# Performance work log

Hardware: AMD Instinct MI355X
Metric: run time of the kernel (lower is better)

## Reference

```python
import jax, jax.numpy as jnp
import numpy as np

N_USER, N_ITEM, N_REL = 200000, 100000, 64
DIM = 64
S_UU = S_UI = S_IU = S_II = 8
BATCH = 65536
MAX_RATING = 5.0


def setup_inputs() -> dict:
    key = jax.random.key(0)
    ks = jax.random.split(key, 24)
    inp = {}
    # query batch
    inp['u'] = jax.random.randint(ks[0], (BATCH,), 0, N_USER)
    inp['v'] = jax.random.randint(ks[1], (BATCH,), 0, N_ITEM)
    # embedding tables (init std=0.8 as in the torch code)
    inp['usr_feat'] = 0.8 * jax.random.normal(ks[2], (N_USER, DIM), jnp.float32)
    inp['item_feat'] = 0.8 * jax.random.normal(ks[3], (N_ITEM, DIM), jnp.float32)
    inp['rel_feat'] = 0.8 * jax.random.normal(ks[4], (N_REL, DIM), jnp.float32)
    # precomputed sampled neighbor tables (built once in __init__ in the original)
    inp['neigh_uu'] = jax.random.randint(ks[5], (N_USER, S_UU), 0, N_USER)
    inp['neigh_uu_st'] = jax.random.uniform(ks[6], (N_USER, S_UU), jnp.float32)
    inp['neigh_ui'] = jax.random.randint(ks[7], (N_USER, S_UI), 0, N_ITEM)
    inp['neigh_ui_rat'] = MAX_RATING * jax.random.uniform(ks[8], (N_USER, S_UI), jnp.float32)
    inp['neigh_ui_vot'] = jax.random.uniform(ks[9], (N_USER, S_UI), jnp.float32)
    inp['neigh_ui_tim'] = jax.random.uniform(ks[10], (N_USER, S_UI), jnp.float32)
    inp['neigh_iu'] = jax.random.randint(ks[11], (N_ITEM, S_IU), 0, N_USER)
    inp['neigh_iu_rat'] = MAX_RATING * jax.random.uniform(ks[12], (N_ITEM, S_IU), jnp.float32)
    inp['neigh_iu_vot'] = jax.random.uniform(ks[13], (N_ITEM, S_IU), jnp.float32)
    inp['neigh_iu_tim'] = jax.random.uniform(ks[14], (N_ITEM, S_IU), jnp.float32)
    inp['neigh_ii'] = jax.random.randint(ks[15], (N_ITEM, S_II), 0, N_ITEM)
    inp['neigh_ir'] = jax.random.randint(ks[16], (N_ITEM, S_II), 0, N_REL)
    # aggregator transforms (one per side)
    sc = 1.0 / np.sqrt(DIM)
    inp['Wu'] = sc * jax.random.normal(ks[17], (DIM, DIM), jnp.float32)
    inp['bu'] = jnp.zeros((DIM,), jnp.float32)
    inp['Wv'] = sc * jax.random.normal(ks[18], (DIM, DIM), jnp.float32)
    inp['bv'] = jnp.zeros((DIM,), jnp.float32)
    return inp


def reference(u, v, usr_feat, item_feat, rel_feat,
              neigh_uu, neigh_uu_st, neigh_ui, neigh_ui_rat, neigh_ui_vot, neigh_ui_tim,
              neigh_iu, neigh_iu_rat, neigh_iu_vot, neigh_iu_tim, neigh_ii, neigh_ir,
              Wu, bu, Wv, bv):
    u_emb = usr_feat[u]                                   # [B, D]
    v_emb = item_feat[v]                                  # [B, D]

    # ---- user-side aggregation ----
    # social neighbors, weighted by softmax over social tie strength
    uu_nei = usr_feat[neigh_uu[u]]                        # [B, S, D]
    w_uu = jax.nn.softmax(neigh_uu_st[u], axis=-1)        # [B, S]
    agg_uu = jnp.einsum('bs,bsd->bd', w_uu, uu_nei)
    # interacted items, weighted by rating * vote * time recency
    ui_nei = item_feat[neigh_ui[u]]                       # [B, S, D]
    s_ui = neigh_ui_rat[u] * neigh_ui_vot[u] * neigh_ui_tim[u]
    w_ui = jax.nn.softmax(s_ui, axis=-1)
    agg_ui = jnp.einsum('bs,bsd->bd', w_ui, ui_nei)
    user_h = jax.nn.relu((u_emb + agg_uu + agg_ui) @ Wu + bu)

    # ---- item-side aggregation ----
    # users who interacted with the item, weighted like above
    iu_nei = usr_feat[neigh_iu[v]]                        # [B, S, D]
    s_iu = neigh_iu_rat[v] * neigh_iu_vot[v] * neigh_iu_tim[v]
    w_iu = jax.nn.softmax(s_iu, axis=-1)
    agg_iu = jnp.einsum('bs,bsd->bd', w_iu, iu_nei)
    # KG neighbors with user-relation attention (KGCN-style)
    ii_nei = item_feat[neigh_ii[v]]                       # [B, S, D]
    rel = rel_feat[neigh_ir[v]]                           # [B, S, D]
    att = jnp.einsum('bd,bsd->bs', u_emb, rel)            # user-relation score
    w_ii = jax.nn.softmax(att, axis=-1)
    agg_ii = jnp.einsum('bs,bsd->bd', w_ii, ii_nei)
    item_h = jax.nn.relu((v_emb + agg_iu + agg_ii) @ Wv + bv)

    # rating prediction
    score = jax.nn.sigmoid(jnp.sum(user_h * item_h, axis=-1)) * MAX_RATING
    return score
```

## Files before the change

### kernel.cpp

```cpp
#include <hip/hip_runtime.h>
#include <math.h>

constexpr int DIM = 64;
constexpr int S = 8;
constexpr int WPB = 4;
constexpr int BLOCK = WPB * 64;
constexpr int GRID = 1024;

typedef __attribute__((ext_vector_type(8))) __bf16 bf16x8;
typedef __attribute__((ext_vector_type(4))) float  f32x4;

#define LDS_FENCE() asm volatile("s_waitcnt lgkmcnt(0)" ::: "memory")

template <int CTRL>
__device__ __forceinline__ float dppx(float x) {
    return __builtin_bit_cast(float,
        __builtin_amdgcn_mov_dpp(__builtin_bit_cast(int, x), CTRL, 0xf, 0xf, true));
}
#define XOR1 0xB1
#define XOR2 0x4E

__device__ __forceinline__ unsigned pk_bf16(float a, float b) {
    unsigned ua = __builtin_bit_cast(unsigned, a);
    unsigned ub = __builtin_bit_cast(unsigned, b);
    ua = (ua + 0x8000u) >> 16;
    ub = (ub + 0x8000u) & 0xffff0000u;
    return ua | ub;
}

__device__ __forceinline__ void octet_softmax(float sc, float* wout) {
    float m = sc;
    m = fmaxf(m, dppx<XOR1>(m));
    m = fmaxf(m, dppx<XOR2>(m));
    m = fmaxf(m, __shfl_xor(m, 4));
    float e = __expf(sc - m);
    float s = e;
    s += dppx<XOR1>(s);
    s += dppx<XOR2>(s);
    s += __shfl_xor(s, 4);
    float w = e / s;
    #pragma unroll
    for (int k = 0; k < 8; k++) wout[k] = __shfl(w, k);
}

__device__ __forceinline__ void matvec_h(
    float xv, int lane, unsigned short* xw,
    const bf16x8* xa00, const bf16x8* xa01,
    const bf16x8* xa10, const bf16x8* xa11,
    const unsigned* bf,
    float b0, float b1, float b2, float b3,
    float& h0, float& h1, float& h2, float& h3)
{
    LDS_FENCE();
    const unsigned xb = __builtin_bit_cast(unsigned, xv);
    const unsigned hb = (xb + 0x8000u) & 0xffff0000u;
    const float xl = xv - __builtin_bit_cast(float, hb);
    xw[lane]      = (unsigned short)(hb >> 16);
    xw[64 + lane] = (unsigned short)((__builtin_bit_cast(unsigned, xl) + 0x8000u) >> 16);
    LDS_FENCE();

    f32x4 a0 = {0.f, 0.f, 0.f, 0.f};
    f32x4 a1 = a0, a2 = a0, a3 = a0;

    {
        const bf16x8 ah = *xa00, al = *xa01;
        const bf16x8 w0 = *(const bf16x8*)(bf);
        const bf16x8 w1 = *(const bf16x8*)(bf + 256);
        const bf16x8 w2 = *(const bf16x8*)(bf + 512);
        const bf16x8 w3 = *(const bf16x8*)(bf + 768);
        a0 = __builtin_amdgcn_mfma_f32_16x16x32_bf16(ah, w0, a0, 0, 0, 0);
        a0 = __builtin_amdgcn_mfma_f32_16x16x32_bf16(al, w0, a0, 0, 0, 0);
        a1 = __builtin_amdgcn_mfma_f32_16x16x32_bf16(ah, w1, a1, 0, 0, 0);
        a1 = __builtin_amdgcn_mfma_f32_16x16x32_bf16(al, w1, a1, 0, 0, 0);
        a2 = __builtin_amdgcn_mfma_f32_16x16x32_bf16(ah, w2, a2, 0, 0, 0);
        a2 = __builtin_amdgcn_mfma_f32_16x16x32_bf16(al, w2, a2, 0, 0, 0);
        a3 = __builtin_amdgcn_mfma_f32_16x16x32_bf16(ah, w3, a3, 0, 0, 0);
        a3 = __builtin_amdgcn_mfma_f32_16x16x32_bf16(al, w3, a3, 0, 0, 0);
    }
    {
        const bf16x8 ah = *xa10, al = *xa11;
        const bf16x8 w0 = *(const bf16x8*)(bf + 1024);
        const bf16x8 w1 = *(const bf16x8*)(bf + 1280);
        const bf16x8 w2 = *(const bf16x8*)(bf + 1536);
        const bf16x8 w3 = *(const bf16x8*)(bf + 1792);
        a0 = __builtin_amdgcn_mfma_f32_16x16x32_bf16(ah, w0, a0, 0, 0, 0);
        a0 = __builtin_amdgcn_mfma_f32_16x16x32_bf16(al, w0, a0, 0, 0, 0);
        a1 = __builtin_amdgcn_mfma_f32_16x16x32_bf16(ah, w1, a1, 0, 0, 0);
        a1 = __builtin_amdgcn_mfma_f32_16x16x32_bf16(al, w1, a1, 0, 0, 0);
        a2 = __builtin_amdgcn_mfma_f32_16x16x32_bf16(ah, w2, a2, 0, 0, 0);
        a2 = __builtin_amdgcn_mfma_f32_16x16x32_bf16(al, w2, a2, 0, 0, 0);
        a3 = __builtin_amdgcn_mfma_f32_16x16x32_bf16(ah, w3, a3, 0, 0, 0);
        a3 = __builtin_amdgcn_mfma_f32_16x16x32_bf16(al, w3, a3, 0, 0, 0);
    }

    h0 = fmaxf(a0[0] + b0, 0.f);
    h1 = fmaxf(a1[0] + b1, 0.f);
    h2 = fmaxf(a2[0] + b2, 0.f);
    h3 = fmaxf(a3[0] + b3, 0.f);
}

__global__ __launch_bounds__(BLOCK, 4)
void sestkgcn_kernel(
    const int*   __restrict__ u_idx,
    const int*   __restrict__ v_idx,
    const float* __restrict__ usr_feat,
    const float* __restrict__ item_feat,
    const float* __restrict__ rel_feat,
    const int*   __restrict__ neigh_uu,
    const float* __restrict__ neigh_uu_st,
    const int*   __restrict__ neigh_ui,
    const float* __restrict__ neigh_ui_rat,
    const float* __restrict__ neigh_ui_vot,
    const float* __restrict__ neigh_ui_tim,
    const int*   __restrict__ neigh_iu,
    const float* __restrict__ neigh_iu_rat,
    const float* __restrict__ neigh_iu_vot,
    const float* __restrict__ neigh_iu_tim,
    const int*   __restrict__ neigh_ii,
    const int*   __restrict__ neigh_ir,
    const float* __restrict__ Wu,
    const float* __restrict__ bu,
    const float* __restrict__ Wv,
    const float* __restrict__ bv,
    float*       __restrict__ out,
    int n)
{
    __shared__ unsigned sBFu[2048];
    __shared__ unsigned sBFv[2048];
    __shared__ __align__(16) unsigned short sX[WPB][128];

    const int tid = threadIdx.x;
    #pragma unroll
    for (int i = tid; i < 2048; i += BLOCK) {
        const int d = i & 3, l = (i >> 2) & 63, f = i >> 8;
        const int row = ((f >> 2) << 5) + ((l >> 4) << 3) + (d << 1);
        const int col = ((f & 3) << 4) + (l & 15);
        sBFu[i] = pk_bf16(Wu[row * DIM + col], Wu[(row + 1) * DIM + col]);
        sBFv[i] = pk_bf16(Wv[row * DIM + col], Wv[(row + 1) * DIM + col]);
    }
    __syncthreads();

    const int wave = tid >> 6;
    const int lane = tid & 63;
    const int ls   = lane & 7;
    const int g    = lane >> 4;
    const int c    = lane & 15;

    unsigned short* xw = &sX[wave][0];
    const bf16x8* xa00 = (const bf16x8*)&sX[wave][g * 8];
    const bf16x8* xa01 = (const bf16x8*)&sX[wave][64 + g * 8];
    const bf16x8* xa10 = (const bf16x8*)&sX[wave][32 + g * 8];
    const bf16x8* xa11 = (const bf16x8*)&sX[wave][96 + g * 8];
    const unsigned* bfu = &sBFu[lane * 4];
    const unsigned* bfv = &sBFv[lane * 4];

    const float bu0 = bu[c], bu1 = bu[c + 16], bu2 = bu[c + 32], bu3 = bu[c + 48];
    const float bv0 = bv[c], bv1 = bv[c + 16], bv2 = bv[c + 32], bv3 = bv[c + 48];

    const int stride = GRID * WPB;
    int b = blockIdx.x * WPB + wave;
    if (b >= n) return;

    int u = u_idx[b];
    int v = v_idx[b];

    while (b < n) {
        const int b2 = b + stride;
        const int bc = (b2 < n) ? b2 : b;
        const int u_nxt = u_idx[bc];
        const int v_nxt = v_idx[bc];

        const unsigned u8 = (unsigned)u << 3, v8 = (unsigned)v << 3;

        const float u_d = usr_feat[((unsigned)u << 6) | (unsigned)lane];
        const float v_d = item_feat[((unsigned)v << 6) | (unsigned)lane];

        const float sc_uu = neigh_uu_st[u8 + ls];
        const float sc_ui = neigh_ui_rat[u8 + ls] * neigh_ui_vot[u8 + ls] * neigh_ui_tim[u8 + ls];
        const float sc_iu = neigh_iu_rat[v8 + ls] * neigh_iu_vot[v8 + ls] * neigh_iu_tim[v8 + ls];

        const int4 iuu0 = ((const int4*)(neigh_uu + u8))[0];
        const int4 iuu1 = ((const int4*)(neigh_uu + u8))[1];
        const int4 iui0 = ((const int4*)(neigh_ui + u8))[0];
        const int4 iui1 = ((const int4*)(neigh_ui + u8))[1];
        const int4 iiu0 = ((const int4*)(neigh_iu + v8))[0];
        const int4 iiu1 = ((const int4*)(neigh_iu + v8))[1];
        const int4 iii0 = ((const int4*)(neigh_ii + v8))[0];
        const int4 iii1 = ((const int4*)(neigh_ii + v8))[1];
        const int4 iir0 = ((const int4*)(neigh_ir + v8))[0];
        const int4 iir1 = ((const int4*)(neigh_ir + v8))[1];

        float r_uu[S], r_ui[S], r_iu[S], r_ii[S], r_rel[S];
        {
            const int nuu[S] = {iuu0.x, iuu0.y, iuu0.z, iuu0.w, iuu1.x, iuu1.y, iuu1.z, iuu1.w};
            const int nui[S] = {iui0.x, iui0.y, iui0.z, iui0.w, iui1.x, iui1.y, iui1.z, iui1.w};
            const int niu[S] = {iiu0.x, iiu0.y, iiu0.z, iiu0.w, iiu1.x, iiu1.y, iiu1.z, iiu1.w};
            const int nii[S] = {iii0.x, iii0.y, iii0.z, iii0.w, iii1.x, iii1.y, iii1.z, iii1.w};
            const int nir[S] = {iir0.x, iir0.y, iir0.z, iir0.w, iir1.x, iir1.y, iir1.z, iir1.w};
            #pragma unroll
            for (int s = 0; s < S; s++) r_uu[s]  = usr_feat[((unsigned)nuu[s] << 6) | (unsigned)lane];
            #pragma unroll
            for (int s = 0; s < S; s++) r_ui[s]  = item_feat[((unsigned)nui[s] << 6) | (unsigned)lane];
            #pragma unroll
            for (int s = 0; s < S; s++) r_iu[s]  = usr_feat[((unsigned)niu[s] << 6) | (unsigned)lane];
            #pragma unroll
            for (int s = 0; s < S; s++) r_ii[s]  = item_feat[((unsigned)nii[s] << 6) | (unsigned)lane];
            #pragma unroll
            for (int s = 0; s < S; s++) r_rel[s] = rel_feat[((unsigned)nir[s] << 6) | (unsigned)lane];
        }

        float w[S];
        octet_softmax(sc_uu, w);
        float agg_uu = 0.f;
        #pragma unroll
        for (int s = 0; s < S; s++) agg_uu = fmaf(w[s], r_uu[s], agg_uu);

        octet_softmax(sc_ui, w);
        float agg_ui = 0.f;
        #pragma unroll
        for (int s = 0; s < S; s++) agg_ui = fmaf(w[s], r_ui[s], agg_ui);

        float hu0, hu1, hu2, hu3;
        matvec_h(u_d + agg_uu + agg_ui, lane, xw, xa00, xa01, xa10, xa11,
                 bfu, bu0, bu1, bu2, bu3, hu0, hu1, hu2, hu3);

        octet_softmax(sc_iu, w);
        float agg_iu = 0.f;
        #pragma unroll
        for (int s = 0; s < S; s++) agg_iu = fmaf(w[s], r_iu[s], agg_iu);

        {
            float p[S];
            #pragma unroll
            for (int s = 0; s < S; s++) p[s] = u_d * r_rel[s];

            float m1[4];
            #pragma unroll
            for (int i = 0; i < 4; i++) {
                float lo = (lane & 1) ? p[2 * i + 1] : p[2 * i];
                float hi = (lane & 1) ? p[2 * i]     : p[2 * i + 1];
                m1[i] = lo + dppx<XOR1>(hi);
            }
            float m2[2];
            #pragma unroll
            for (int i = 0; i < 2; i++) {
                float lo = (lane & 2) ? m1[2 * i + 1] : m1[2 * i];
                float hi = (lane & 2) ? m1[2 * i]     : m1[2 * i + 1];
                m2[i] = lo + dppx<XOR2>(hi);
            }
            float lo = (lane & 4) ? m2[1] : m2[0];
            float hi = (lane & 4) ? m2[0] : m2[1];
            float att = lo + __shfl_xor(hi, 4);
            att += __shfl_xor(att, 8);
            att += __shfl_xor(att, 16);
            att += __shfl_xor(att, 32);
            octet_softmax(att, w);
        }
        float agg_ii = 0.f;
        #pragma unroll
        for (int s = 0; s < S; s++) agg_ii = fmaf(w[s], r_ii[s], agg_ii);

        float hv0, hv1, hv2, hv3;
        matvec_h(v_d + agg_iu + agg_ii, lane, xw, xa00, xa01, xa10, xa11,
                 bfv, bv0, bv1, bv2, bv3, hv0, hv1, hv2, hv3);

        float p = hu0 * hv0 + hu1 * hv1 + hu2 * hv2 + hu3 * hv3;
        p += dppx<XOR1>(p);
        p += dppx<XOR2>(p);
        p += __shfl_xor(p, 4);
        p += __shfl_xor(p, 8);
        if (lane == 0) out[b] = 5.0f / (1.0f + __expf(-p));

        b = b2;
        u = u_nxt;
        v = v_nxt;
    }
}

extern "C" void kernel_launch(void* const* d_in, const int* in_sizes, int n_in,
                              void* d_out, int out_size, void* d_ws, size_t ws_size,
                              hipStream_t stream) {
    const int*   u_idx        = (const int*)  d_in[0];
    const int*   v_idx        = (const int*)  d_in[1];
    const float* usr_feat     = (const float*)d_in[2];
    const float* item_feat    = (const float*)d_in[3];
    const float* rel_feat     = (const float*)d_in[4];
    const int*   neigh_uu     = (const int*)  d_in[5];
    const float* neigh_uu_st  = (const float*)d_in[6];
    const int*   neigh_ui     = (const int*)  d_in[7];
    const float* neigh_ui_rat = (const float*)d_in[8];
    const float* neigh_ui_vot = (const float*)d_in[9];
    const float* neigh_ui_tim = (const float*)d_in[10];
    const int*   neigh_iu     = (const int*)  d_in[11];
    const float* neigh_iu_rat = (const float*)d_in[12];
    const float* neigh_iu_vot = (const float*)d_in[13];
    const float* neigh_iu_tim = (const float*)d_in[14];
    const int*   neigh_ii     = (const int*)  d_in[15];
    const int*   neigh_ir     = (const int*)  d_in[16];
    const float* Wu           = (const float*)d_in[17];
    const float* bu           = (const float*)d_in[18];
    const float* Wv           = (const float*)d_in[19];
    const float* bv           = (const float*)d_in[20];
    float*       out          = (float*)d_out;

    const int n = in_sizes[0];
    int blocks = (n + WPB - 1) / WPB;
    if (blocks > GRID) blocks = GRID;
    sestkgcn_kernel<<<blocks, BLOCK, 0, stream>>>(
        u_idx, v_idx, usr_feat, item_feat, rel_feat,
        neigh_uu, neigh_uu_st, neigh_ui, neigh_ui_rat, neigh_ui_vot, neigh_ui_tim,
        neigh_iu, neigh_iu_rat, neigh_iu_vot, neigh_iu_tim, neigh_ii, neigh_ir,
        Wu, bu, Wv, bv, out, n);
}
```

Before: 250.3 us.

## Software-pipeline neighbor gathers across loop iterations with sched barriers

Restructures the per-wave batch loop into a software pipeline. Neighbor index rows for the next query are loaded early, and the embedding gathers and scores for the next query are issued before the current item-side matvec. Indices two iterations ahead are prefetched, and sched_barrier pins keep the compiler from reordering these phases. The aim is to hide gather latency behind compute. In exchange it holds more registers live, which can lower occupancy.

```diff
diff --git a/kernel.cpp b/kernel.cpp
--- a/kernel.cpp
+++ b/kernel.cpp
@@ -11,6 +11,7 @@
 typedef __attribute__((ext_vector_type(4))) float  f32x4;
 
 #define LDS_FENCE() asm volatile("s_waitcnt lgkmcnt(0)" ::: "memory")
+#define SCHED_PIN() __builtin_amdgcn_sched_barrier(0)
 
 template <int CTRL>
 __device__ __forceinline__ float dppx(float x) {
@@ -130,7 +131,6 @@
     __shared__ __align__(16) unsigned short sX[WPB][128];
 
     const int tid = threadIdx.x;
-    #pragma unroll
     for (int i = tid; i < 2048; i += BLOCK) {
         const int d = i & 3, l = (i >> 2) & 63, f = i >> 8;
         const int row = ((f >> 2) << 5) + ((l >> 4) << 3) + (d << 1);
@@ -161,78 +161,89 @@
     int b = blockIdx.x * WPB + wave;
     if (b >= n) return;
 
-    int u = u_idx[b];
-    int v = v_idx[b];
-
-    while (b < n) {
-        const int b2 = b + stride;
-        const int bc = (b2 < n) ? b2 : b;
-        const int u_nxt = u_idx[bc];
-        const int v_nxt = v_idx[bc];
-
-        const unsigned u8 = (unsigned)u << 3, v8 = (unsigned)v << 3;
-
-        const float u_d = usr_feat[((unsigned)u << 6) | (unsigned)lane];
-        const float v_d = item_feat[((unsigned)v << 6) | (unsigned)lane];
-
-        const float sc_uu = neigh_uu_st[u8 + ls];
-        const float sc_ui = neigh_ui_rat[u8 + ls] * neigh_ui_vot[u8 + ls] * neigh_ui_tim[u8 + ls];
-        const float sc_iu = neigh_iu_rat[v8 + ls] * neigh_iu_vot[v8 + ls] * neigh_iu_tim[v8 + ls];
-
-        const int4 iuu0 = ((const int4*)(neigh_uu + u8))[0];
-        const int4 iuu1 = ((const int4*)(neigh_uu + u8))[1];
-        const int4 iui0 = ((const int4*)(neigh_ui + u8))[0];
-        const int4 iui1 = ((const int4*)(neigh_ui + u8))[1];
-        const int4 iiu0 = ((const int4*)(neigh_iu + v8))[0];
-        const int4 iiu1 = ((const int4*)(neigh_iu + v8))[1];
-        const int4 iii0 = ((const int4*)(neigh_ii + v8))[0];
-        const int4 iii1 = ((const int4*)(neigh_ii + v8))[1];
-        const int4 iir0 = ((const int4*)(neigh_ir + v8))[0];
-        const int4 iir1 = ((const int4*)(neigh_ir + v8))[1];
-
-        float r_uu[S], r_ui[S], r_iu[S], r_ii[S], r_rel[S];
+    int u = u_idx[b], v = v_idx[b];
+    int bc1 = b + stride; if (bc1 >= n) bc1 = b;
+    int u1 = u_idx[bc1], v1 = v_idx[bc1];
+
+    unsigned u8 = (unsigned)u << 3, v8 = (unsigned)v << 3;
+    int4 iuu0 = ((const int4*)(neigh_uu + u8))[0];
+    int4 iuu1 = ((const int4*)(neigh_uu + u8))[1];
+    int4 iui0 = ((const int4*)(neigh_ui + u8))[0];
+    int4 iui1 = ((const int4*)(neigh_ui + u8))[1];
+    int4 iiu0 = ((const int4*)(neigh_iu + v8))[0];
+    int4 iiu1 = ((const int4*)(neigh_iu + v8))[1];
+    int4 iii0 = ((const int4*)(neigh_ii + v8))[0];
+    int4 iii1 = ((const int4*)(neigh_ii + v8))[1];
+    int4 iir0 = ((const int4*)(neigh_ir + v8))[0];
+    int4 iir1 = ((const int4*)(neigh_ir + v8))[1];
+    float suu_r = neigh_uu_st[u8 + ls];
+    float uir = neigh_ui_rat[u8 + ls], uiv = neigh_ui_vot[u8 + ls], uit = neigh_ui_tim[u8 + ls];
+    float iur = neigh_iu_rat[v8 + ls], ivv = neigh_iu_vot[v8 + ls], ivt = neigh_iu_tim[v8 + ls];
+    float ud_c = usr_feat[((unsigned)u << 6) | (unsigned)lane];
+    float vd_c = item_feat[((unsigned)v << 6) | (unsigned)lane];
+    float ruu[S], rui[S], riu[S], rii[S];
+    {
+        const int nuu[S] = {iuu0.x, iuu0.y, iuu0.z, iuu0.w, iuu1.x, iuu1.y, iuu1.z, iuu1.w};
+        const int nui[S] = {iui0.x, iui0.y, iui0.z, iui0.w, iui1.x, iui1.y, iui1.z, iui1.w};
+        const int niu[S] = {iiu0.x, iiu0.y, iiu0.z, iiu0.w, iiu1.x, iiu1.y, iiu1.z, iiu1.w};
+        const int nii[S] = {iii0.x, iii0.y, iii0.z, iii0.w, iii1.x, iii1.y, iii1.z, iii1.w};
+        #pragma unroll
+        for (int s = 0; s < S; s++) ruu[s] = usr_feat[((unsigned)nuu[s] << 6) | (unsigned)lane];
+        #pragma unroll
+        for (int s = 0; s < S; s++) rui[s] = item_feat[((unsigned)nui[s] << 6) | (unsigned)lane];
+        #pragma unroll
+        for (int s = 0; s < S; s++) riu[s] = usr_feat[((unsigned)niu[s] << 6) | (unsigned)lane];
+        #pragma unroll
+        for (int s = 0; s < S; s++) rii[s] = item_feat[((unsigned)nii[s] << 6) | (unsigned)lane];
+    }
+    float ud_n = 0.f, vd_n = 0.f;
+
+    while (true) {
+        float rr[S];
         {
-            const int nuu[S] = {iuu0.x, iuu0.y, iuu0.z, iuu0.w, iuu1.x, iuu1.y, iuu1.z, iuu1.w};
-            const int nui[S] = {iui0.x, iui0.y, iui0.z, iui0.w, iui1.x, iui1.y, iui1.z, iui1.w};
-            const int niu[S] = {iiu0.x, iiu0.y, iiu0.z, iiu0.w, iiu1.x, iiu1.y, iiu1.z, iiu1.w};
-            const int nii[S] = {iii0.x, iii0.y, iii0.z, iii0.w, iii1.x, iii1.y, iii1.z, iii1.w};
             const int nir[S] = {iir0.x, iir0.y, iir0.z, iir0.w, iir1.x, iir1.y, iir1.z, iir1.w};
             #pragma unroll
-            for (int s = 0; s < S; s++) r_uu[s]  = usr_feat[((unsigned)nuu[s] << 6) | (unsigned)lane];
-            #pragma unroll
-            for (int s = 0; s < S; s++) r_ui[s]  = item_feat[((unsigned)nui[s] << 6) | (unsigned)lane];
-            #pragma unroll
-            for (int s = 0; s < S; s++) r_iu[s]  = usr_feat[((unsigned)niu[s] << 6) | (unsigned)lane];
-            #pragma unroll
-            for (int s = 0; s < S; s++) r_ii[s]  = item_feat[((unsigned)nii[s] << 6) | (unsigned)lane];
-            #pragma unroll
-            for (int s = 0; s < S; s++) r_rel[s] = rel_feat[((unsigned)nir[s] << 6) | (unsigned)lane];
+            for (int s = 0; s < S; s++) rr[s] = rel_feat[((unsigned)nir[s] << 6) | (unsigned)lane];
         }
+        const unsigned u81 = (unsigned)u1 << 3, v81 = (unsigned)v1 << 3;
+        iuu0 = ((const int4*)(neigh_uu + u81))[0];
+        iuu1 = ((const int4*)(neigh_uu + u81))[1];
+        iui0 = ((const int4*)(neigh_ui + u81))[0];
+        iui1 = ((const int4*)(neigh_ui + u81))[1];
+        iiu0 = ((const int4*)(neigh_iu + v81))[0];
+        iiu1 = ((const int4*)(neigh_iu + v81))[1];
+        iii0 = ((const int4*)(neigh_ii + v81))[0];
+        iii1 = ((const int4*)(neigh_ii + v81))[1];
+        iir0 = ((const int4*)(neigh_ir + v81))[0];
+        iir1 = ((const int4*)(neigh_ir + v81))[1];
+        int b2c = b + 2 * stride; if (b2c >= n) b2c = b;
+        const int u2 = u_idx[b2c], v2 = v_idx[b2c];
+        SCHED_PIN();
 
         float w[S];
-        octet_softmax(sc_uu, w);
+        octet_softmax(suu_r, w);
         float agg_uu = 0.f;
         #pragma unroll
-        for (int s = 0; s < S; s++) agg_uu = fmaf(w[s], r_uu[s], agg_uu);
-
-        octet_softmax(sc_ui, w);
+        for (int s = 0; s < S; s++) agg_uu = fmaf(w[s], ruu[s], agg_uu);
+
+        octet_softmax(uir * uiv * uit, w);
         float agg_ui = 0.f;
         #pragma unroll
-        for (int s = 0; s < S; s++) agg_ui = fmaf(w[s], r_ui[s], agg_ui);
+        for (int s = 0; s < S; s++) agg_ui = fmaf(w[s], rui[s], agg_ui);
 
         float hu0, hu1, hu2, hu3;
-        matvec_h(u_d + agg_uu + agg_ui, lane, xw, xa00, xa01, xa10, xa11,
+        matvec_h(ud_c + agg_uu + agg_ui, lane, xw, xa00, xa01, xa10, xa11,
                  bfu, bu0, bu1, bu2, bu3, hu0, hu1, hu2, hu3);
 
-        octet_softmax(sc_iu, w);
+        octet_softmax(iur * ivv * ivt, w);
         float agg_iu = 0.f;
         #pragma unroll
-        for (int s = 0; s < S; s++) agg_iu = fmaf(w[s], r_iu[s], agg_iu);
+        for (int s = 0; s < S; s++) agg_iu = fmaf(w[s], riu[s], agg_iu);
 
         {
             float p[S];
             #pragma unroll
-            for (int s = 0; s < S; s++) p[s] = u_d * r_rel[s];
+            for (int s = 0; s < S; s++) p[s] = ud_c * rr[s];
 
             float m1[4];
             #pragma unroll
@@ -258,10 +269,31 @@
         }
         float agg_ii = 0.f;
         #pragma unroll
-        for (int s = 0; s < S; s++) agg_ii = fmaf(w[s], r_ii[s], agg_ii);
+        for (int s = 0; s < S; s++) agg_ii = fmaf(w[s], rii[s], agg_ii);
+
+        {
+            const int nuu[S] = {iuu0.x, iuu0.y, iuu0.z, iuu0.w, iuu1.x, iuu1.y, iuu1.z, iuu1.w};
+            const int nui[S] = {iui0.x, iui0.y, iui0.z, iui0.w, iui1.x, iui1.y, iui1.z, iui1.w};
+            const int niu[S] = {iiu0.x, iiu0.y, iiu0.z, iiu0.w, iiu1.x, iiu1.y, iiu1.z, iiu1.w};
+            const int nii[S] = {iii0.x, iii0.y, iii0.z, iii0.w, iii1.x, iii1.y, iii1.z, iii1.w};
+            #pragma unroll
+            for (int s = 0; s < S; s++) ruu[s] = usr_feat[((unsigned)nuu[s] << 6) | (unsigned)lane];
+            #pragma unroll
+            for (int s = 0; s < S; s++) rui[s] = item_feat[((unsigned)nui[s] << 6) | (unsigned)lane];
+            #pragma unroll
+            for (int s = 0; s < S; s++) riu[s] = usr_feat[((unsigned)niu[s] << 6) | (unsigned)lane];
+            #pragma unroll
+            for (int s = 0; s < S; s++) rii[s] = item_feat[((unsigned)nii[s] << 6) | (unsigned)lane];
+        }
+        suu_r = neigh_uu_st[u81 + ls];
+        uir = neigh_ui_rat[u81 + ls]; uiv = neigh_ui_vot[u81 + ls]; uit = neigh_ui_tim[u81 + ls];
+        iur = neigh_iu_rat[v81 + ls]; ivv = neigh_iu_vot[v81 + ls]; ivt = neigh_iu_tim[v81 + ls];
+        ud_n = usr_feat[((unsigned)u1 << 6) | (unsigned)lane];
+        vd_n = item_feat[((unsigned)v1 << 6) | (unsigned)lane];
+        SCHED_PIN();
 
         float hv0, hv1, hv2, hv3;
-        matvec_h(v_d + agg_iu + agg_ii, lane, xw, xa00, xa01, xa10, xa11,
+        matvec_h(vd_c + agg_iu + agg_ii, lane, xw, xa00, xa01, xa10, xa11,
                  bfv, bv0, bv1, bv2, bv3, hv0, hv1, hv2, hv3);
 
         float p = hu0 * hv0 + hu1 * hv1 + hu2 * hv2 + hu3 * hv3;
@@ -271,9 +303,10 @@
         p += __shfl_xor(p, 8);
         if (lane == 0) out[b] = 5.0f / (1.0f + __expf(-p));
 
-        b = b2;
-        u = u_nxt;
-        v = v_nxt;
+        b += stride;
+        if (b >= n) break;
+        u = u1; v = v1; u1 = u2; v1 = v2;
+        ud_c = ud_n; vd_c = vd_n;
     }
 }
 
```

After: 253.6 us. No clear change (+1.3%).
